# Optimization experiments

Hardware: AMD Instinct MI355X
Metric: run time of the kernel (lower is better)

The kernel has to match this reference:

```python
import jax, jax.numpy as jnp
import numpy as np

N = 50000          # number of nodes / output rows (len(degs))
IN_C, OUT_C = 16, 16
EDGE_F = 13        # edge feature dim fed to filter net
HID = 32           # filter-net hidden width
E_NOMINAL = 800000 # target number of edges (sum of degs)


def setup_inputs() -> dict:
    rng = np.random.default_rng(0)
    # variable per-node degrees in [0, 32], adjusted so they sum exactly to E_NOMINAL
    degs = rng.integers(0, 33, size=N).astype(np.int64)
    degs[0] = max(0, degs[0] + (E_NOMINAL - int(degs.sum())))
    E = int(degs.sum())
    # segment id of each edge = destination node (equivalent to the degs-driven loop)
    idxd = np.repeat(np.arange(N, dtype=np.int32), degs)
    idxn = rng.integers(0, N, size=E).astype(np.int32)  # source node gather index

    key = jax.random.key(0)
    k1, k2, k3, k4 = jax.random.split(key, 4)
    x = jax.random.normal(k1, (N, IN_C), jnp.float32)
    edgefeats = jax.random.normal(k2, (E, EDGE_F), jnp.float32)
    # filter net: Linear(EDGE_F->HID) -> ReLU -> Linear(HID->IN_C*OUT_C)
    W1 = jax.random.normal(k3, (EDGE_F, HID), jnp.float32) / np.float32(np.sqrt(EDGE_F))
    b1 = jnp.zeros((HID,), jnp.float32)
    W2 = jax.random.normal(k4, (HID, IN_C * OUT_C), jnp.float32) / np.float32(np.sqrt(HID))
    b2 = jnp.zeros((IN_C * OUT_C,), jnp.float32)
    return {
        "x": x, "edgefeats": edgefeats,
        "W1": W1, "b1": b1, "W2": W2, "b2": b2,
        "idxn": jnp.asarray(idxn), "idxd": jnp.asarray(idxd),
        "degs": jnp.asarray(degs.astype(np.float32)),
    }


def reference(x, edgefeats, W1, b1, W2, b2, idxn, idxd, degs):
    # filter net generates a per-edge [IN_C, OUT_C] weight matrix
    h = jax.nn.relu(edgefeats @ W1 + b1)                 # [E, HID]
    w = (h @ W2 + b2).reshape(-1, IN_C, OUT_C)           # [E, IN_C, OUT_C]
    # gather source-node features and apply per-edge matvec (bmm with [E,1,IN_C])
    sel = x[idxn]                                        # [E, IN_C]
    prod = jnp.einsum('ei,eio->eo', sel, w)              # [E, OUT_C]
    # segment-mean over each node's incoming edges; degree-0 nodes -> 0
    s = jax.ops.segment_sum(prod, idxd, num_segments=N)  # [N, OUT_C]
    d = degs[:, None]
    return jnp.where(d > 0, s / jnp.maximum(d, 1.0), jnp.float32(0.0))
```

## Files before the change

kernel.cpp:

```cpp
#include <hip/hip_runtime.h>

typedef _Float16 half2v __attribute__((ext_vector_type(2)));
typedef _Float16 half4v __attribute__((ext_vector_type(4)));
typedef _Float16 half8v __attribute__((ext_vector_type(8)));
typedef float   float4v __attribute__((ext_vector_type(4)));

#define INC     16
#define OUTC    16
#define EFN     13
#define HIDC    32
#define EPB     128
#define NTILES  (EPB / 16)
#define MAXSPAN 80

union H8 { half8v v; half2v h2[4]; };

__global__ __launch_bounds__(256) void pack_w2(const float* __restrict__ W2,
                                               _Float16* __restrict__ wsB)
{
    const int i = blockIdx.x * 256 + threadIdx.x;
    const int j = i & 7;
    const int l = (i >> 3) & 63;
    const int t = i >> 9;
    const int q = l >> 4, n = l & 15;
    const int kk = (j < 4) ? (q * 4 + j) : (16 + q * 4 + (j & 3));
    wsB[i] = (_Float16)W2[kk * 256 + t * 16 + n];
}

__global__ __launch_bounds__(64, 3) void edge_kernel(
    const float* __restrict__ x,
    const float* __restrict__ edgefeats,
    const float* __restrict__ W1,
    const float* __restrict__ b1,
    const float* __restrict__ b2,
    const int*   __restrict__ idxn,
    const int*   __restrict__ idxd,
    const float* __restrict__ degs,
    const _Float16* __restrict__ wsB,
    float*       __restrict__ out,
    float*       __restrict__ wsPfirst,
    float*       __restrict__ wsPlast,
    int*         __restrict__ wsMeta,
    int E)
{
    __shared__ float lacc[MAXSPAN * OUTC];
    __shared__ __align__(4) unsigned char su[EPB];

    const int lane = threadIdx.x;
    const int n    = lane & 15;
    const int q    = lane >> 4;

    const long b0   = (long)blockIdx.x * EPB;
    const long bEnd = (b0 + EPB < (long)E) ? (b0 + EPB) : (long)E;
    const int  d_lo = idxd[b0];
    const int  d_hi = idxd[bEnd - 1];
    const int  span = d_hi - d_lo;

    H8 bfr[16];
    #pragma unroll
    for (int t = 0; t < 16; ++t)
        bfr[t].v = *(const half8v*)(wsB + ((size_t)(t * 64 + lane) * 8));

    #pragma unroll
    for (int it = 0; it < MAXSPAN * OUTC / 64; ++it) lacc[lane + it * 64] = 0.0f;
    {
        const int i2 = lane * 2;
        long e0 = b0 + i2, e1 = b0 + i2 + 1;
        if (e0 >= (long)E) e0 = E - 1;
        if (e1 >= (long)E) e1 = E - 1;
        const unsigned u0 = (unsigned)(idxd[e0] - d_lo);
        const unsigned u1 = (unsigned)(idxd[e1] - d_lo);
        *(unsigned short*)&su[i2] = (unsigned short)(u0 | (u1 << 8));
    }

    half4v a1, a2;
    float4v c1, c2;
    #pragma unroll
    for (int jj = 0; jj < 4; ++jj) {
        const int f = q * 4 + jj;
        const bool ok = (f < EFN);
        a1[jj] = ok ? (_Float16)W1[f * HIDC + n]      : (_Float16)0.f;
        a2[jj] = ok ? (_Float16)W1[f * HIDC + 16 + n] : (_Float16)0.f;
        c1[jj] = b1[q * 4 + jj];
        c2[jj] = b1[16 + q * 4 + jj];
    }
    half8v bfragB2;
    #pragma unroll
    for (int j = 0; j < 8; ++j) {
        _Float16 val = (_Float16)0.f;
        if (q < 2) val = (_Float16)b2[(q * 8 + j) * 16 + n];
        bfragB2[j] = val;
    }

    const int f0 = (q < 3) ? (q * 4) : 9;

    __syncthreads();

    const int ntile_blk = (int)((bEnd - b0 + 15) >> 4);
    long e0n = b0 + n;
    int nodeN = idxn[(e0n < (long)E) ? e0n : (long)(E - 1)];

    for (int t16 = 0; t16 < ntile_blk; ++t16) {
        const long base = b0 + (long)t16 * 16;
        const long eM   = base + n;
        const bool vM   = (eM < (long)E);
        const long eMc  = vM ? eM : (long)(E - 1);

        const int node = nodeN;
        {
            const long en = base + 16 + n;
            nodeN = idxn[(en < (long)E) ? en : (long)(E - 1)];
        }

        const unsigned u4 = *(const unsigned*)&su[t16 * 16 + q * 4];

        const float4 ef4 = *(const float4*)(edgefeats + (size_t)eMc * EFN + f0);

        const float4* xp = (const float4*)(x + (size_t)node * INC);
        float4 s0 = xp[0], s1 = xp[1], s2 = xp[2], s3 = xp[3];
        if (!vM) { s0 = make_float4(0,0,0,0); s1 = s0; s2 = s0; s3 = s0; }

        half2v selh[8];
        { half2v t = {(_Float16)s0.x, (_Float16)s0.y}; selh[0] = t; }
        { half2v t = {(_Float16)s0.z, (_Float16)s0.w}; selh[1] = t; }
        { half2v t = {(_Float16)s1.x, (_Float16)s1.y}; selh[2] = t; }
        { half2v t = {(_Float16)s1.z, (_Float16)s1.w}; selh[3] = t; }
        { half2v t = {(_Float16)s2.x, (_Float16)s2.y}; selh[4] = t; }
        { half2v t = {(_Float16)s2.z, (_Float16)s2.w}; selh[5] = t; }
        { half2v t = {(_Float16)s3.x, (_Float16)s3.y}; selh[6] = t; }
        { half2v t = {(_Float16)s3.z, (_Float16)s3.w}; selh[7] = t; }

        half4v efB;
        if (q < 3) {
            efB[0] = (_Float16)ef4.x; efB[1] = (_Float16)ef4.y;
            efB[2] = (_Float16)ef4.z; efB[3] = (_Float16)ef4.w;
        } else {
            efB[0] = (_Float16)ef4.w; efB[1] = (_Float16)0.f;
            efB[2] = (_Float16)0.f;   efB[3] = (_Float16)0.f;
        }

        const float4v hf1 = __builtin_amdgcn_mfma_f32_16x16x16f16(a1, efB, c1, 0, 0, 0);
        const float4v hf2 = __builtin_amdgcn_mfma_f32_16x16x16f16(a2, efB, c2, 0, 0, 0);

        H8 hu;
        #pragma unroll
        for (int r = 0; r < 2; ++r) {
            half2v t1 = {(_Float16)fmaxf(hf1[2*r], 0.f), (_Float16)fmaxf(hf1[2*r+1], 0.f)};
            half2v t2 = {(_Float16)fmaxf(hf2[2*r], 0.f), (_Float16)fmaxf(hf2[2*r+1], 0.f)};
            hu.h2[r]     = t1;
            hu.h2[2 + r] = t2;
        }

        float4v acc = {0.f, 0.f, 0.f, 0.f};
        #pragma unroll
        for (int t = 0; t < 16; ++t) {
            _Float16 sv = (t & 1) ? selh[t >> 1][1] : selh[t >> 1][0];
            half2v sb = {sv, sv};
            H8 a;
            a.h2[0] = sb * hu.h2[0];
            a.h2[1] = sb * hu.h2[1];
            a.h2[2] = sb * hu.h2[2];
            a.h2[3] = sb * hu.h2[3];
            acc = __builtin_amdgcn_mfma_f32_16x16x32_f16(a.v, bfr[t].v, acc, 0, 0, 0);
        }
        {
            H8 a;
            #pragma unroll
            for (int j2 = 0; j2 < 4; ++j2) {
                half2v zz = {(_Float16)0.f, (_Float16)0.f};
                a.h2[j2] = (q < 2) ? selh[q * 4 + j2] : zz;
            }
            acc = __builtin_amdgcn_mfma_f32_16x16x32_f16(a.v, bfragB2, acc, 0, 0, 0);
        }

        const unsigned rep = (u4 & 0xffu) * 0x01010101u;
        if (u4 == rep) {
            atomicAdd(&lacc[(u4 & 0xffu) * OUTC + n],
                      acc[0] + acc[1] + acc[2] + acc[3]);
        } else {
            #pragma unroll
            for (int r = 0; r < 4; ++r)
                atomicAdd(&lacc[((u4 >> (8 * r)) & 0xffu) * OUTC + n], acc[r]);
        }
    }

    __syncthreads();

    const bool first_starts = (b0 == 0)        || (idxd[b0 - 1] != d_lo);
    const bool last_ends    = (bEnd == (long)E) || (idxd[bEnd]   != d_hi);

    for (int i = lane; i < (span + 1) * OUTC; i += 64) {
        const int u = i >> 4;
        const int o = i & 15;
        const int v = d_lo + u;
        const float bin = lacc[u * OUTC + o];
        const bool starts = (u > 0)    || first_starts;
        const bool ends   = (u < span) || last_ends;
        if (starts && ends) {
            const float dg = degs[v];
            out[(size_t)v * OUTC + o] = (dg > 0.0f) ? bin / dg : 0.0f;
        } else if (!starts) {
            wsPfirst[(size_t)blockIdx.x * OUTC + o] = bin;
        } else {
            wsPlast[(size_t)blockIdx.x * OUTC + o] = bin;
        }
    }
    if (lane == 0) {
        wsMeta[blockIdx.x * 4 + 0] = d_hi;
        wsMeta[blockIdx.x * 4 + 1] = last_ends ? 1 : 0;
        wsMeta[blockIdx.x * 4 + 2] =
            (((span > 0) || first_starts) && !last_ends) ? 1 : 0;
    }
}

__global__ __launch_bounds__(256) void fixup_kernel(
    const float* __restrict__ degs,
    float*       __restrict__ out,
    const float* __restrict__ wsPfirst,
    const float* __restrict__ wsPlast,
    const int*   __restrict__ wsMeta,
    int N, int nblocks)
{
    const int t = blockIdx.x * 256 + threadIdx.x;

    if (t < nblocks && wsMeta[t * 4 + 2]) {
        const int v = wsMeta[t * 4 + 0];
        float tot[OUTC];
        #pragma unroll
        for (int o = 0; o < OUTC; ++o) tot[o] = wsPlast[(size_t)t * OUTC + o];
        for (int j = t + 1; j < nblocks; ++j) {
            #pragma unroll
            for (int o = 0; o < OUTC; ++o) tot[o] += wsPfirst[(size_t)j * OUTC + o];
            if (wsMeta[j * 4 + 0] != v || wsMeta[j * 4 + 1]) break;
        }
        const float dg = degs[v];
        #pragma unroll
        for (int o = 0; o < OUTC; ++o) out[(size_t)v * OUTC + o] = tot[o] / dg;
    }

    if (t < N && degs[t] == 0.0f) {
        float4* op = (float4*)(out + (size_t)t * OUTC);
        const float4 z = make_float4(0, 0, 0, 0);
        op[0] = z; op[1] = z; op[2] = z; op[3] = z;
    }
}

extern "C" void kernel_launch(void* const* d_in, const int* in_sizes, int n_in,
                              void* d_out, int out_size, void* d_ws, size_t ws_size,
                              hipStream_t stream)
{
    const float* x         = (const float*)d_in[0];
    const float* edgefeats = (const float*)d_in[1];
    const float* W1        = (const float*)d_in[2];
    const float* b1        = (const float*)d_in[3];
    const float* W2        = (const float*)d_in[4];
    const float* b2        = (const float*)d_in[5];
    const int*   idxn      = (const int*)d_in[6];
    const int*   idxd      = (const int*)d_in[7];
    const float* degs      = (const float*)d_in[8];

    const int E = in_sizes[6];
    const int N = in_sizes[8];
    const int nblocks = (E + EPB - 1) / EPB;

    _Float16* wsB    = (_Float16*)d_ws;
    float* wsPfirst  = (float*)((char*)d_ws + 16384);
    float* wsPlast   = wsPfirst + (size_t)nblocks * OUTC;
    int*   wsMeta    = (int*)(wsPlast + (size_t)nblocks * OUTC);

    pack_w2<<<32, 256, 0, stream>>>(W2, wsB);

    edge_kernel<<<nblocks, 64, 0, stream>>>(x, edgefeats, W1, b1, b2,
                                            idxn, idxd, degs, wsB, (float*)d_out,
                                            wsPfirst, wsPlast, wsMeta, E);

    const int fthreads = (N > nblocks) ? N : nblocks;
    fixup_kernel<<<(fthreads + 255) / 256, 256, 0, stream>>>(
        degs, (float*)d_out, wsPfirst, wsPlast, wsMeta, N, nblocks);
}
```

Baseline: 163.8 us.

## Pre-convert x to fp16 and software-pipeline gathers one tile ahead

Measured after the change: 167.8 us. 1.02x slower.

```diff
diff --git a/kernel.cpp b/kernel.cpp
--- a/kernel.cpp
+++ b/kernel.cpp
@@ -10,25 +10,43 @@
 #define EFN     13
 #define HIDC    32
 #define EPB     128
-#define NTILES  (EPB / 16)
 #define MAXSPAN 80
 
 union H8 { half8v v; half2v h2[4]; };
 
-__global__ __launch_bounds__(256) void pack_w2(const float* __restrict__ W2,
-                                               _Float16* __restrict__ wsB)
+__global__ __launch_bounds__(256) void prep(
+    const float* __restrict__ W2,
+    const float* __restrict__ x,
+    _Float16*    __restrict__ wsB,
+    _Float16*    __restrict__ wsXh,
+    int nh)
 {
-    const int i = blockIdx.x * 256 + threadIdx.x;
-    const int j = i & 7;
-    const int l = (i >> 3) & 63;
-    const int t = i >> 9;
-    const int q = l >> 4, n = l & 15;
-    const int kk = (j < 4) ? (q * 4 + j) : (16 + q * 4 + (j & 3));
-    wsB[i] = (_Float16)W2[kk * 256 + t * 16 + n];
+    const int b = blockIdx.x;
+    if (b < 32) {
+        const int i = b * 256 + threadIdx.x;
+        const int j = i & 7;
+        const int l = (i >> 3) & 63;
+        const int t = i >> 9;
+        const int q = l >> 4, n = l & 15;
+        const int kk = (j < 4) ? (q * 4 + j) : (16 + q * 4 + (j & 3));
+        wsB[i] = (_Float16)W2[kk * 256 + t * 16 + n];
+    } else {
+        const int i = (b - 32) * 256 + threadIdx.x;
+        if (i * 8 < nh) {
+            const float4 v0 = ((const float4*)x)[i * 2];
+            const float4 v1 = ((const float4*)x)[i * 2 + 1];
+            half8v h;
+            h[0] = (_Float16)v0.x; h[1] = (_Float16)v0.y;
+            h[2] = (_Float16)v0.z; h[3] = (_Float16)v0.w;
+            h[4] = (_Float16)v1.x; h[5] = (_Float16)v1.y;
+            h[6] = (_Float16)v1.z; h[7] = (_Float16)v1.w;
+            *(half8v*)(wsXh + (size_t)i * 8) = h;
+        }
+    }
 }
 
-__global__ __launch_bounds__(64, 3) void edge_kernel(
-    const float* __restrict__ x,
+__global__ __launch_bounds__(64, 4) void edge_kernel(
+    const _Float16* __restrict__ xh,
     const float* __restrict__ edgefeats,
     const float* __restrict__ W1,
     const float* __restrict__ b1,
@@ -97,45 +115,46 @@
     __syncthreads();
 
     const int ntile_blk = (int)((bEnd - b0 + 15) >> 4);
+
+    const long Em1 = (long)E - 1;
     long e0n = b0 + n;
-    int nodeN = idxn[(e0n < (long)E) ? e0n : (long)(E - 1)];
+    const int node0 = idxn[(e0n < (long)E) ? e0n : Em1];
+    int nodeN = idxn[(e0n + 16 < (long)E) ? (e0n + 16) : Em1];
+    half8v xA = *(const half8v*)(xh + (size_t)node0 * INC);
+    half8v xB = *(const half8v*)(xh + (size_t)node0 * INC + 8);
+    long ec0 = (e0n < (long)E) ? e0n : Em1;
+    float4 efc = *(const float4*)(edgefeats + (size_t)ec0 * EFN + f0);
 
     for (int t16 = 0; t16 < ntile_blk; ++t16) {
         const long base = b0 + (long)t16 * 16;
-        const long eM   = base + n;
-        const bool vM   = (eM < (long)E);
-        const long eMc  = vM ? eM : (long)(E - 1);
-
-        const int node = nodeN;
-        {
-            const long en = base + 16 + n;
-            nodeN = idxn[(en < (long)E) ? en : (long)(E - 1)];
-        }
+        const bool vM   = (base + n < (long)E);
+
+        const long en2 = base + 32 + n;
+        const int nodeN2 = idxn[(en2 < (long)E) ? en2 : Em1];
+        const half8v xA1 = *(const half8v*)(xh + (size_t)nodeN * INC);
+        const half8v xB1 = *(const half8v*)(xh + (size_t)nodeN * INC + 8);
+        const long en1 = base + 16 + n;
+        const long en1c = (en1 < (long)E) ? en1 : Em1;
+        const float4 ef1 = *(const float4*)(edgefeats + (size_t)en1c * EFN + f0);
 
         const unsigned u4 = *(const unsigned*)&su[t16 * 16 + q * 4];
 
-        const float4 ef4 = *(const float4*)(edgefeats + (size_t)eMc * EFN + f0);
-
-        const float4* xp = (const float4*)(x + (size_t)node * INC);
-        float4 s0 = xp[0], s1 = xp[1], s2 = xp[2], s3 = xp[3];
-        if (!vM) { s0 = make_float4(0,0,0,0); s1 = s0; s2 = s0; s3 = s0; }
-
+        H8 sa, sb_;
+        sa.v = xA; sb_.v = xB;
+        const half2v zz = {(_Float16)0.f, (_Float16)0.f};
         half2v selh[8];
-        { half2v t = {(_Float16)s0.x, (_Float16)s0.y}; selh[0] = t; }
-        { half2v t = {(_Float16)s0.z, (_Float16)s0.w}; selh[1] = t; }
-        { half2v t = {(_Float16)s1.x, (_Float16)s1.y}; selh[2] = t; }
-        { half2v t = {(_Float16)s1.z, (_Float16)s1.w}; selh[3] = t; }
-        { half2v t = {(_Float16)s2.x, (_Float16)s2.y}; selh[4] = t; }
-        { half2v t = {(_Float16)s2.z, (_Float16)s2.w}; selh[5] = t; }
-        { half2v t = {(_Float16)s3.x, (_Float16)s3.y}; selh[6] = t; }
-        { half2v t = {(_Float16)s3.z, (_Float16)s3.w}; selh[7] = t; }
+        #pragma unroll
+        for (int i = 0; i < 4; ++i) {
+            selh[i]     = vM ? sa.h2[i]  : zz;
+            selh[4 + i] = vM ? sb_.h2[i] : zz;
+        }
 
         half4v efB;
         if (q < 3) {
-            efB[0] = (_Float16)ef4.x; efB[1] = (_Float16)ef4.y;
-            efB[2] = (_Float16)ef4.z; efB[3] = (_Float16)ef4.w;
+            efB[0] = (_Float16)efc.x; efB[1] = (_Float16)efc.y;
+            efB[2] = (_Float16)efc.z; efB[3] = (_Float16)efc.w;
         } else {
-            efB[0] = (_Float16)ef4.w; efB[1] = (_Float16)0.f;
+            efB[0] = (_Float16)efc.w; efB[1] = (_Float16)0.f;
             efB[2] = (_Float16)0.f;   efB[3] = (_Float16)0.f;
         }
 
@@ -167,7 +186,6 @@
             H8 a;
             #pragma unroll
             for (int j2 = 0; j2 < 4; ++j2) {
-                half2v zz = {(_Float16)0.f, (_Float16)0.f};
                 a.h2[j2] = (q < 2) ? selh[q * 4 + j2] : zz;
             }
             acc = __builtin_amdgcn_mfma_f32_16x16x32_f16(a.v, bfragB2, acc, 0, 0, 0);
@@ -182,6 +200,10 @@
             for (int r = 0; r < 4; ++r)
                 atomicAdd(&lacc[((u4 >> (8 * r)) & 0xffu) * OUTC + n], acc[r]);
         }
+
+        nodeN = nodeN2;
+        xA = xA1; xB = xB1;
+        efc = ef1;
     }
 
     __syncthreads();
@@ -262,15 +284,19 @@
     const int E = in_sizes[6];
     const int N = in_sizes[8];
     const int nblocks = (E + EPB - 1) / EPB;
-
-    _Float16* wsB    = (_Float16*)d_ws;
-    float* wsPfirst  = (float*)((char*)d_ws + 16384);
-    float* wsPlast   = wsPfirst + (size_t)nblocks * OUTC;
-    int*   wsMeta    = (int*)(wsPlast + (size_t)nblocks * OUTC);
-
-    pack_w2<<<32, 256, 0, stream>>>(W2, wsB);
-
-    edge_kernel<<<nblocks, 64, 0, stream>>>(x, edgefeats, W1, b1, b2,
+    const int nh = N * INC;
+
+    _Float16* wsB  = (_Float16*)d_ws;
+    _Float16* wsXh = (_Float16*)((char*)d_ws + 16384);
+    size_t xh_bytes = ((size_t)nh * 2 + 255) & ~(size_t)255;
+    float* wsPfirst = (float*)((char*)d_ws + 16384 + xh_bytes);
+    float* wsPlast  = wsPfirst + (size_t)nblocks * OUTC;
+    int*   wsMeta   = (int*)(wsPlast + (size_t)nblocks * OUTC);
+
+    const int xhblocks = (nh / 8 + 255) / 256;
+    prep<<<32 + xhblocks, 256, 0, stream>>>(W2, x, wsB, wsXh, nh);
+
+    edge_kernel<<<nblocks, 64, 0, stream>>>(wsXh, edgefeats, W1, b1, b2,
                                             idxn, idxd, degs, wsB, (float*)d_out,
                                             wsPfirst, wsPlast, wsMeta, E);
 
```
